# Optimization experiments

Measured on AMD Instinct MI355X. Metric: run time of the kernel, lower is better.

The kernel has to match this reference:

```python
import jax, jax.numpy as jnp
import numpy as np

B, Q, V, H, U = 4, 256, 2048, 512, 128

def setup_inputs() -> dict:
    key = jax.random.key(0)
    ks = jax.random.split(key, 5)
    return {
        "queries": jax.random.normal(ks[0], (B, Q, H), dtype=jnp.float32),
        "values": jax.random.normal(ks[1], (B, V, H), dtype=jnp.float32),
        "w1": jax.random.normal(ks[2], (H, U), dtype=jnp.float32) / np.sqrt(H),
        "w2": jax.random.normal(ks[3], (H, U), dtype=jnp.float32) / np.sqrt(H),
        "v": jax.random.normal(ks[4], (U,), dtype=jnp.float32) / np.sqrt(U),
    }

def reference(queries, values, w1, w2, v):
    # Project queries and values first (cheap GEMMs), then broadcast-add.
    pq = jnp.einsum("bqh,hu->bqu", queries, w1)          # [B,Q,U]
    pv = jnp.einsum("bvh,hu->bvu", values, w2)           # [B,V,U]
    # added_qv: [B,Q,V,U] -- the large intermediate the original materializes
    scores = jnp.einsum("bqvu,u->bqv", jnp.tanh(pq[:, :, None, :] + pv[:, None, :, :]), v)
    attn = jax.nn.softmax(scores, axis=-1)               # softmax over V (last axis, as tf.nn.softmax)
    return jnp.einsum("bqv,bvh->bqh", attn, values)      # [B,Q,H]
```

## Files before the change

### kernel.cpp

```cpp
#include <hip/hip_runtime.h>

#define BB 4
#define QQ 256
#define VV 2048
#define HH 512
#define UU 128

#define C2E   2.8853900817779268f
#define LOG2E 1.4426950408889634f

__device__ __forceinline__ void fma4(float4& a, float s, const float4& w) {
    a.x = fmaf(s, w.x, a.x);
    a.y = fmaf(s, w.y, a.y);
    a.z = fmaf(s, w.z, a.z);
    a.w = fmaf(s, w.w, a.w);
}
__device__ __forceinline__ float2 rcp2(float2 x) {
    return make_float2(__builtin_amdgcn_rcpf(x.x), __builtin_amdgcn_rcpf(x.y));
}
__device__ __forceinline__ float2 mul2(float2 a, float2 b) { return make_float2(a.x*b.x, a.y*b.y); }
__device__ __forceinline__ float2 muls(float2 a, float s)  { return make_float2(a.x*s, a.y*s); }
__device__ __forceinline__ float2 fma2(float2 a, float2 b, float2 c) {
    return make_float2(fmaf(a.x, b.x, c.x), fmaf(a.y, b.y, c.y));
}
__device__ __forceinline__ float2 fmas(float2 a, float s, float2 c) {
    return make_float2(fmaf(a.x, s, c.x), fmaf(a.y, s, c.y));
}

__global__ __launch_bounds__(256) void proj_kernel(const float* __restrict__ queries,
                                                   const float* __restrict__ values,
                                                   const float* __restrict__ w1,
                                                   const float* __restrict__ w2,
                                                   float* __restrict__ pqI,
                                                   float* __restrict__ pvI,
                                                   float* __restrict__ denom) {
    __shared__ float smem[32 * 36 + 32 * 128];
    float (*As)[36] = (float(*)[36])smem;
    float* Ws = smem + 32 * 36;
    float (*Ls)[36] = (float(*)[36])smem;

    const int bid = blockIdx.x;
    const int tid = threadIdx.x;
    if (bid == 0) *(float4*)&denom[tid * 4] = make_float4(0.f, 0.f, 0.f, 0.f);

    const bool isv = (bid < 256);
    const float* A; const float* W; int b, r0, ROWS; float* Ob;
    if (isv) {
        b = bid >> 6; r0 = (bid & 63) * 32;
        A = values + ((size_t)(b * VV + r0)) * HH;  W = w2;
        Ob = pvI + (size_t)b * UU * VV;  ROWS = VV;
    } else {
        const int q = bid - 256;
        b = q >> 3; r0 = (q & 7) * 32;
        A = queries + ((size_t)(b * QQ + r0)) * HH; W = w1;
        Ob = pqI + (size_t)b * UU * QQ;  ROWS = QQ;
    }

    const int tx = tid & 31;
    const int ty = tid >> 5;
    float4 acc[4];
#pragma unroll
    for (int j = 0; j < 4; j++) acc[j] = make_float4(0.f, 0.f, 0.f, 0.f);

    for (int k0 = 0; k0 < HH; k0 += 32) {
        {
            const int r = tid >> 3, kk4 = (tid & 7) * 4;
            const float4 a = *(const float4*)&A[(size_t)r * HH + k0 + kk4];
            As[kk4 + 0][r] = a.x; As[kk4 + 1][r] = a.y;
            As[kk4 + 2][r] = a.z; As[kk4 + 3][r] = a.w;
        }
#pragma unroll
        for (int t = 0; t < 4; t++) {
            const int f = tid + t * 256;
            const int kk = f >> 5, u4 = (f & 31) * 4;
            *(float4*)&Ws[kk * 128 + u4] = *(const float4*)&W[(size_t)(k0 + kk) * UU + u4];
        }
        __syncthreads();
#pragma unroll
        for (int kk = 0; kk < 32; kk++) {
            const float4 a = *(const float4*)&As[kk][ty * 4];
            const float4 w = *(const float4*)&Ws[kk * 128 + tx * 4];
            fma4(acc[0], a.x, w);
            fma4(acc[1], a.y, w);
            fma4(acc[2], a.z, w);
            fma4(acc[3], a.w, w);
        }
        __syncthreads();
    }
#pragma unroll
    for (int j = 0; j < 4; j++) {
        const float aa[4] = {acc[j].x, acc[j].y, acc[j].z, acc[j].w};
#pragma unroll
        for (int i = 0; i < 4; i++)
            Ls[tx * 4 + i][ty * 4 + j] = __builtin_amdgcn_exp2f(aa[i] * C2E);
    }
    __syncthreads();
#pragma unroll
    for (int t = 0; t < 4; t++) {
        const int idx = tid + t * 256;
        const int g = idx >> 5, r = idx & 31;
        float4 o;
        o.x = Ls[4 * g + 0][r]; o.y = Ls[4 * g + 1][r];
        o.z = Ls[4 * g + 2][r]; o.w = Ls[4 * g + 3][r];
        *(float4*)&Ob[((size_t)g * ROWS + r0 + r) * 4] = o;
    }
}

__global__ __launch_bounds__(1024, 4) void fused_kernel(const float* __restrict__ pqI,
                                                        const float* __restrict__ pvI,
                                                        const float* __restrict__ vvec,
                                                        const float* __restrict__ values,
                                                        float* __restrict__ slab,
                                                        float* __restrict__ denom) {
    __shared__ float att[512][20];
    __shared__ float scratch[24 * 512];
    __shared__ float wred[8][16];
    const int tid = threadIdx.x;
    const int bid = blockIdx.x;
    const int vs = bid & 3, qb = (bid >> 2) & 15, b = bid >> 6;
    const int qbase = qb * 16, vbase = vs * 512;

    const int vloc = tid & 511;
    const int uh = tid >> 9;
    const int v = vbase + vloc;

    float vsum = 0.0f;
#pragma unroll
    for (int u4 = 0; u4 < UU; u4 += 4) {
        const float4 t = *(const float4*)&vvec[u4];
        vsum += t.x + t.y + t.z + t.w;
    }

    const float* pv4 = pvI + (size_t)b * UU * VV + (size_t)v * 4;
    const float* pq4 = pqI + (size_t)b * UU * QQ + (size_t)qbase * 4;

    float2 acc[8];
#pragma unroll
    for (int p = 0; p < 8; p++) acc[p] = make_float2(0.f, 0.f);

    const int G0 = uh * 16;
    float4 ev = *(const float4*)&pv4[(size_t)G0 * VV * 4];

    for (int g = 0; g < 16; g++) {
        const int G = G0 + g;
        const float* eqp = &pq4[(size_t)G * QQ * 4];
        float4 e[16];
#pragma unroll
        for (int i = 0; i < 16; i++)
            e[i] = *(const float4*)&eqp[i * 4];
        float4 evn;
        if (g < 15) evn = *(const float4*)&pv4[(size_t)(G + 1) * VV * 4];
        const float4 wq = *(const float4*)&vvec[G * 4];
        const float w0 = 2.f * wq.x, w1 = 2.f * wq.y;
        const float w2 = 2.f * wq.z, w3 = 2.f * wq.w;
#pragma unroll
        for (int p = 0; p < 8; p++) {
            const float4 e0 = e[2 * p];
            const float4 e1 = e[2 * p + 1];
            const float2 a1 = make_float2(fmaf(e0.x, ev.x, 1.f), fmaf(e1.x, ev.x, 1.f));
            const float2 b1 = make_float2(fmaf(e0.y, ev.y, 1.f), fmaf(e1.y, ev.y, 1.f));
            const float2 c1 = make_float2(fmaf(e0.z, ev.z, 1.f), fmaf(e1.z, ev.z, 1.f));
            const float2 d1 = make_float2(fmaf(e0.w, ev.w, 1.f), fmaf(e1.w, ev.w, 1.f));
            const float2 pab = mul2(a1, b1), pcd = mul2(c1, d1);
            const float2 nab = fmas(a1, w1, muls(b1, w0));
            const float2 ncd = fmas(c1, w3, muls(d1, w2));
            const float2 num = fma2(nab, pcd, mul2(ncd, pab));
            const float2 den = mul2(pab, pcd);
            acc[p] = fma2(num, rcp2(den), acc[p]);
        }
        ev = evn;
    }

    float* cb = scratch;
    if (uh == 1) {
#pragma unroll
        for (int p = 0; p < 8; p++) {
            cb[(2 * p + 0) * 512 + vloc] = acc[p].x;
            cb[(2 * p + 1) * 512 + vloc] = acc[p].y;
        }
    }
    __syncthreads();
    if (uh == 0) {
#pragma unroll
        for (int p = 0; p < 8; p++) {
            const float hx = cb[(2 * p + 0) * 512 + vloc];
            const float hy = cb[(2 * p + 1) * 512 + vloc];
            float2 e;
            e.x = __builtin_amdgcn_exp2f((vsum - (acc[p].x + hx)) * LOG2E);
            e.y = __builtin_amdgcn_exp2f((vsum - (acc[p].y + hy)) * LOG2E);
            *(float2*)&att[vloc][2 * p] = e;
            acc[p] = e;
        }
#pragma unroll
        for (int off = 1; off < 64; off <<= 1) {
#pragma unroll
            for (int p = 0; p < 8; p++) {
                acc[p].x += __shfl_xor(acc[p].x, off, 64);
                acc[p].y += __shfl_xor(acc[p].y, off, 64);
            }
        }
        if ((tid & 63) == 0) {
            const int w = tid >> 6;
#pragma unroll
            for (int p = 0; p < 8; p++) {
                wred[w][2 * p + 0] = acc[p].x;
                wred[w][2 * p + 1] = acc[p].y;
            }
        }
    }
    __syncthreads();
    if (tid < 16) {
        float s = 0.f;
#pragma unroll
        for (int w = 0; w < 8; w++) s += wred[w][tid];
        atomicAdd(&denom[b * QQ + qbase + tid], s);
    }

    const int hg = tid & 127, sel = tid >> 7;
    const int qh = sel & 1, vh = sel >> 1;
    const int h0 = hg * 4;
    const float* vp = values + ((size_t)(b * VV + vbase + vh * 128)) * HH + h0;

    float4 oacc[8];
#pragma unroll
    for (int j = 0; j < 8; j++) oacc[j] = make_float4(0.f, 0.f, 0.f, 0.f);

#pragma unroll 2
    for (int vv = 0; vv < 128; vv++) {
        const float4 w = *(const float4*)&vp[(size_t)vv * HH];
        const float4 a0 = *(const float4*)&att[vh * 128 + vv][qh * 8 + 0];
        const float4 a1 = *(const float4*)&att[vh * 128 + vv][qh * 8 + 4];
        fma4(oacc[0], a0.x, w); fma4(oacc[1], a0.y, w);
        fma4(oacc[2], a0.z, w); fma4(oacc[3], a0.w, w);
        fma4(oacc[4], a1.x, w); fma4(oacc[5], a1.y, w);
        fma4(oacc[6], a1.z, w); fma4(oacc[7], a1.w, w);
    }

    float (*scr)[512] = (float(*)[512])scratch;
    for (int rr = 0; rr < 2; rr++) {
        __syncthreads();
        if (qh == rr && vh > 0) {
#pragma unroll
            for (int j = 0; j < 8; j++)
                *(float4*)&scr[(vh - 1) * 8 + j][h0] = oacc[j];
        }
        __syncthreads();
        if (qh == rr && vh == 0) {
            float* sp = slab + (size_t)vs * (BB * QQ * HH);
#pragma unroll
            for (int j = 0; j < 8; j++) {
                const float4 p0 = *(const float4*)&scr[0 * 8 + j][h0];
                const float4 p1 = *(const float4*)&scr[1 * 8 + j][h0];
                const float4 p2 = *(const float4*)&scr[2 * 8 + j][h0];
                float4 o;
                o.x = oacc[j].x + p0.x + p1.x + p2.x;
                o.y = oacc[j].y + p0.y + p1.y + p2.y;
                o.z = oacc[j].z + p0.z + p1.z + p2.z;
                o.w = oacc[j].w + p0.w + p1.w + p2.w;
                *(float4*)&sp[((size_t)(b * QQ + qbase + rr * 8 + j)) * HH + h0] = o;
            }
        }
    }
}

__global__ __launch_bounds__(256) void reduce_kernel(const float* __restrict__ slab,
                                                     const float* __restrict__ denom,
                                                     float* __restrict__ out) {
    const int i = blockIdx.x * 256 + threadIdx.x;
    const float r = __builtin_amdgcn_rcpf(denom[i >> 7]);
    const float4* s4 = (const float4*)slab;
    float4 s = s4[i];
#pragma unroll
    for (int k = 1; k < 4; k++) {
        const float4 p = s4[(size_t)k * (BB * QQ * HH / 4) + i];
        s.x += p.x; s.y += p.y; s.z += p.z; s.w += p.w;
    }
    s.x *= r; s.y *= r; s.z *= r; s.w *= r;
    ((float4*)out)[i] = s;
}

extern "C" void kernel_launch(void* const* d_in, const int* in_sizes, int n_in,
                              void* d_out, int out_size, void* d_ws, size_t ws_size,
                              hipStream_t stream) {
    const float* queries = (const float*)d_in[0];
    const float* values  = (const float*)d_in[1];
    const float* w1      = (const float*)d_in[2];
    const float* w2      = (const float*)d_in[3];
    const float* vvec    = (const float*)d_in[4];
    float* out = (float*)d_out;

    float* ws    = (float*)d_ws;
    float* pqI   = ws;
    float* pvI   = pqI + BB * UU * QQ;
    float* denom = pvI + (size_t)BB * UU * VV;
    float* slab  = denom + BB * QQ;

    proj_kernel<<<256 + 32, 256, 0, stream>>>(queries, values, w1, w2, pqI, pvI, denom);
    fused_kernel<<<BB * (QQ / 16) * (VV / 512), 1024, 0, stream>>>(pqI, pvI, vvec, values, slab, denom);
    reduce_kernel<<<(BB * QQ * HH) / 4 / 256, 256, 0, stream>>>(slab, denom, out);
}
```

Baseline: 175.2 us.

## Split fused attention kernel into separate scores and PV kernels

After: 231.6 us. 32.2% more time.

```diff
diff --git a/kernel.cpp b/kernel.cpp
--- a/kernel.cpp
+++ b/kernel.cpp
@@ -106,25 +106,18 @@
     }
 }
 
-__global__ __launch_bounds__(1024, 4) void fused_kernel(const float* __restrict__ pqI,
+__global__ __launch_bounds__(256, 8) void scores_kernel(const float* __restrict__ pqI,
                                                         const float* __restrict__ pvI,
                                                         const float* __restrict__ vvec,
-                                                        const float* __restrict__ values,
-                                                        float* __restrict__ slab,
+                                                        float* __restrict__ attT,
                                                         float* __restrict__ denom) {
-    __shared__ float att[512][20];
-    __shared__ float scratch[24 * 512];
-    __shared__ float wred[8][16];
-    const int tid = threadIdx.x;
-    const int bid = blockIdx.x;
-    const int vs = bid & 3, qb = (bid >> 2) & 15, b = bid >> 6;
-    const int qbase = qb * 16, vbase = vs * 512;
-
-    const int vloc = tid & 511;
-    const int uh = tid >> 9;
-    const int v = vbase + vloc;
-
-    float vsum = 0.0f;
+    const int tid = threadIdx.x, bid = blockIdx.x;
+    const int lane = tid & 63, w = tid >> 6;
+    const int vb = bid & 31, qb = (bid >> 5) & 15, b = bid >> 9;
+    const int v = vb * 64 + lane;
+    const int q0 = qb * 16 + w * 4;
+
+    float vsum = 0.f;
 #pragma unroll
     for (int u4 = 0; u4 < UU; u4 += 4) {
         const float4 t = *(const float4*)&vvec[u4];
@@ -132,31 +125,24 @@
     }
 
     const float* pv4 = pvI + (size_t)b * UU * VV + (size_t)v * 4;
-    const float* pq4 = pqI + (size_t)b * UU * QQ + (size_t)qbase * 4;
-
-    float2 acc[8];
-#pragma unroll
-    for (int p = 0; p < 8; p++) acc[p] = make_float2(0.f, 0.f);
-
-    const int G0 = uh * 16;
-    float4 ev = *(const float4*)&pv4[(size_t)G0 * VV * 4];
-
-    for (int g = 0; g < 16; g++) {
-        const int G = G0 + g;
+    const float* pq4 = pqI + (size_t)b * UU * QQ + (size_t)q0 * 4;
+
+    float2 acc[2];
+    acc[0] = make_float2(0.f, 0.f);
+    acc[1] = make_float2(0.f, 0.f);
+
+    float4 ev = *(const float4*)&pv4[0];
+    for (int G = 0; G < 32; G++) {
+        float4 evn;
+        if (G < 31) evn = *(const float4*)&pv4[(size_t)(G + 1) * VV * 4];
         const float* eqp = &pq4[(size_t)G * QQ * 4];
-        float4 e[16];
-#pragma unroll
-        for (int i = 0; i < 16; i++)
-            e[i] = *(const float4*)&eqp[i * 4];
-        float4 evn;
-        if (g < 15) evn = *(const float4*)&pv4[(size_t)(G + 1) * VV * 4];
         const float4 wq = *(const float4*)&vvec[G * 4];
         const float w0 = 2.f * wq.x, w1 = 2.f * wq.y;
         const float w2 = 2.f * wq.z, w3 = 2.f * wq.w;
 #pragma unroll
-        for (int p = 0; p < 8; p++) {
-            const float4 e0 = e[2 * p];
-            const float4 e1 = e[2 * p + 1];
+        for (int p = 0; p < 2; p++) {
+            const float4 e0 = *(const float4*)&eqp[(2 * p) * 4];
+            const float4 e1 = *(const float4*)&eqp[(2 * p + 1) * 4];
             const float2 a1 = make_float2(fmaf(e0.x, ev.x, 1.f), fmaf(e1.x, ev.x, 1.f));
             const float2 b1 = make_float2(fmaf(e0.y, ev.y, 1.f), fmaf(e1.y, ev.y, 1.f));
             const float2 c1 = make_float2(fmaf(e0.z, ev.z, 1.f), fmaf(e1.z, ev.z, 1.f));
@@ -171,55 +157,43 @@
         ev = evn;
     }
 
-    float* cb = scratch;
-    if (uh == 1) {
-#pragma unroll
-        for (int p = 0; p < 8; p++) {
-            cb[(2 * p + 0) * 512 + vloc] = acc[p].x;
-            cb[(2 * p + 1) * 512 + vloc] = acc[p].y;
-        }
-    }
-    __syncthreads();
-    if (uh == 0) {
-#pragma unroll
-        for (int p = 0; p < 8; p++) {
-            const float hx = cb[(2 * p + 0) * 512 + vloc];
-            const float hy = cb[(2 * p + 1) * 512 + vloc];
-            float2 e;
-            e.x = __builtin_amdgcn_exp2f((vsum - (acc[p].x + hx)) * LOG2E);
-            e.y = __builtin_amdgcn_exp2f((vsum - (acc[p].y + hy)) * LOG2E);
-            *(float2*)&att[vloc][2 * p] = e;
-            acc[p] = e;
-        }
-#pragma unroll
-        for (int off = 1; off < 64; off <<= 1) {
-#pragma unroll
-            for (int p = 0; p < 8; p++) {
-                acc[p].x += __shfl_xor(acc[p].x, off, 64);
-                acc[p].y += __shfl_xor(acc[p].y, off, 64);
-            }
-        }
-        if ((tid & 63) == 0) {
-            const int w = tid >> 6;
-#pragma unroll
-            for (int p = 0; p < 8; p++) {
-                wred[w][2 * p + 0] = acc[p].x;
-                wred[w][2 * p + 1] = acc[p].y;
-            }
-        }
-    }
-    __syncthreads();
-    if (tid < 16) {
-        float s = 0.f;
-#pragma unroll
-        for (int w = 0; w < 8; w++) s += wred[w][tid];
-        atomicAdd(&denom[b * QQ + qbase + tid], s);
-    }
+    float4 eo;
+    eo.x = __builtin_amdgcn_exp2f((vsum - acc[0].x) * LOG2E);
+    eo.y = __builtin_amdgcn_exp2f((vsum - acc[0].y) * LOG2E);
+    eo.z = __builtin_amdgcn_exp2f((vsum - acc[1].x) * LOG2E);
+    eo.w = __builtin_amdgcn_exp2f((vsum - acc[1].y) * LOG2E);
+    *(float4*)&attT[((((size_t)b * 16 + qb) * VV) + v) * 16 + w * 4] = eo;
+
+    float4 s = eo;
+#pragma unroll
+    for (int off = 1; off < 64; off <<= 1) {
+        s.x += __shfl_xor(s.x, off, 64);
+        s.y += __shfl_xor(s.y, off, 64);
+        s.z += __shfl_xor(s.z, off, 64);
+        s.w += __shfl_xor(s.w, off, 64);
+    }
+    if (lane == 0) {
+        atomicAdd(&denom[b * QQ + q0 + 0], s.x);
+        atomicAdd(&denom[b * QQ + q0 + 1], s.y);
+        atomicAdd(&denom[b * QQ + q0 + 2], s.z);
+        atomicAdd(&denom[b * QQ + q0 + 3], s.w);
+    }
+}
+
+__global__ __launch_bounds__(1024, 4) void pv_kernel(const float* __restrict__ attT,
+                                                     const float* __restrict__ values,
+                                                     float* __restrict__ slab) {
+    __shared__ float scratch[24 * 512];
+    const int tid = threadIdx.x;
+    const int bid = blockIdx.x;
+    const int vs = bid & 3, qb = (bid >> 2) & 15, b = bid >> 6;
+    const int qbase = qb * 16, vbase = vs * 512;
 
     const int hg = tid & 127, sel = tid >> 7;
     const int qh = sel & 1, vh = sel >> 1;
     const int h0 = hg * 4;
     const float* vp = values + ((size_t)(b * VV + vbase + vh * 128)) * HH + h0;
+    const float* ap = attT + (((size_t)b * 16 + qb) * VV + vbase + vh * 128) * 16;
 
     float4 oacc[8];
 #pragma unroll
@@ -228,8 +202,8 @@
 #pragma unroll 2
     for (int vv = 0; vv < 128; vv++) {
         const float4 w = *(const float4*)&vp[(size_t)vv * HH];
-        const float4 a0 = *(const float4*)&att[vh * 128 + vv][qh * 8 + 0];
-        const float4 a1 = *(const float4*)&att[vh * 128 + vv][qh * 8 + 4];
+        const float4 a0 = *(const float4*)&ap[vv * 16 + qh * 8 + 0];
+        const float4 a1 = *(const float4*)&ap[vv * 16 + qh * 8 + 4];
         fma4(oacc[0], a0.x, w); fma4(oacc[1], a0.y, w);
         fma4(oacc[2], a0.z, w); fma4(oacc[3], a0.w, w);
         fma4(oacc[4], a1.x, w); fma4(oacc[5], a1.y, w);
@@ -294,8 +268,10 @@
     float* pvI   = pqI + BB * UU * QQ;
     float* denom = pvI + (size_t)BB * UU * VV;
     float* slab  = denom + BB * QQ;
+    float* attT  = slab + (size_t)4 * (BB * QQ * HH);
 
     proj_kernel<<<256 + 32, 256, 0, stream>>>(queries, values, w1, w2, pqI, pvI, denom);
-    fused_kernel<<<BB * (QQ / 16) * (VV / 512), 1024, 0, stream>>>(pqI, pvI, vvec, values, slab, denom);
+    scores_kernel<<<BB * (QQ / 16) * (VV / 64), 256, 0, stream>>>(pqI, pvI, vvec, attT, denom);
+    pv_kernel<<<BB * (QQ / 16) * (VV / 512), 1024, 0, stream>>>(attT, values, slab);
     reduce_kernel<<<(BB * QQ * HH) / 4 / 256, 256, 0, stream>>>(slab, denom, out);
 }
```

## Fuse projection, attention and reduction into one cooperative kernel with grid syncs

Applied to the files above, without the earlier changes.

Measured after the change: 271.6 us. 55.1% more time.

```diff
diff --git a/kernel.cpp b/kernel.cpp
--- a/kernel.cpp
+++ b/kernel.cpp
@@ -1,4 +1,5 @@
 #include <hip/hip_runtime.h>
+#include <hip/hip_cooperative_groups.h>
 
 #define BB 4
 #define QQ 256
@@ -27,256 +28,265 @@
     return make_float2(fmaf(a.x, s, c.x), fmaf(a.y, s, c.y));
 }
 
-__global__ __launch_bounds__(256) void proj_kernel(const float* __restrict__ queries,
-                                                   const float* __restrict__ values,
-                                                   const float* __restrict__ w1,
-                                                   const float* __restrict__ w2,
-                                                   float* __restrict__ pqI,
-                                                   float* __restrict__ pvI,
-                                                   float* __restrict__ denom) {
-    __shared__ float smem[32 * 36 + 32 * 128];
-    float (*As)[36] = (float(*)[36])smem;
-    float* Ws = smem + 32 * 36;
-    float (*Ls)[36] = (float(*)[36])smem;
-
-    const int bid = blockIdx.x;
-    const int tid = threadIdx.x;
-    if (bid == 0) *(float4*)&denom[tid * 4] = make_float4(0.f, 0.f, 0.f, 0.f);
-
-    const bool isv = (bid < 256);
-    const float* A; const float* W; int b, r0, ROWS; float* Ob;
-    if (isv) {
-        b = bid >> 6; r0 = (bid & 63) * 32;
-        A = values + ((size_t)(b * VV + r0)) * HH;  W = w2;
-        Ob = pvI + (size_t)b * UU * VV;  ROWS = VV;
-    } else {
-        const int q = bid - 256;
-        b = q >> 3; r0 = (q & 7) * 32;
-        A = queries + ((size_t)(b * QQ + r0)) * HH; W = w1;
-        Ob = pqI + (size_t)b * UU * QQ;  ROWS = QQ;
-    }
-
-    const int tx = tid & 31;
-    const int ty = tid >> 5;
-    float4 acc[4];
-#pragma unroll
-    for (int j = 0; j < 4; j++) acc[j] = make_float4(0.f, 0.f, 0.f, 0.f);
-
-    for (int k0 = 0; k0 < HH; k0 += 32) {
-        {
-            const int r = tid >> 3, kk4 = (tid & 7) * 4;
-            const float4 a = *(const float4*)&A[(size_t)r * HH + k0 + kk4];
-            As[kk4 + 0][r] = a.x; As[kk4 + 1][r] = a.y;
-            As[kk4 + 2][r] = a.z; As[kk4 + 3][r] = a.w;
-        }
-#pragma unroll
-        for (int t = 0; t < 4; t++) {
-            const int f = tid + t * 256;
-            const int kk = f >> 5, u4 = (f & 31) * 4;
-            *(float4*)&Ws[kk * 128 + u4] = *(const float4*)&W[(size_t)(k0 + kk) * UU + u4];
-        }
-        __syncthreads();
-#pragma unroll
-        for (int kk = 0; kk < 32; kk++) {
-            const float4 a = *(const float4*)&As[kk][ty * 4];
-            const float4 w = *(const float4*)&Ws[kk * 128 + tx * 4];
-            fma4(acc[0], a.x, w);
-            fma4(acc[1], a.y, w);
-            fma4(acc[2], a.z, w);
-            fma4(acc[3], a.w, w);
-        }
-        __syncthreads();
-    }
-#pragma unroll
-    for (int j = 0; j < 4; j++) {
-        const float aa[4] = {acc[j].x, acc[j].y, acc[j].z, acc[j].w};
-#pragma unroll
-        for (int i = 0; i < 4; i++)
-            Ls[tx * 4 + i][ty * 4 + j] = __builtin_amdgcn_exp2f(aa[i] * C2E);
-    }
-    __syncthreads();
-#pragma unroll
-    for (int t = 0; t < 4; t++) {
-        const int idx = tid + t * 256;
-        const int g = idx >> 5, r = idx & 31;
-        float4 o;
-        o.x = Ls[4 * g + 0][r]; o.y = Ls[4 * g + 1][r];
-        o.z = Ls[4 * g + 2][r]; o.w = Ls[4 * g + 3][r];
-        *(float4*)&Ob[((size_t)g * ROWS + r0 + r) * 4] = o;
-    }
-}
-
-__global__ __launch_bounds__(1024, 4) void fused_kernel(const float* __restrict__ pqI,
-                                                        const float* __restrict__ pvI,
-                                                        const float* __restrict__ vvec,
-                                                        const float* __restrict__ values,
-                                                        float* __restrict__ slab,
-                                                        float* __restrict__ denom) {
+__global__ __launch_bounds__(1024, 4) void mega_kernel(const float* __restrict__ queries,
+                                                       const float* __restrict__ values,
+                                                       const float* __restrict__ w1,
+                                                       const float* __restrict__ w2,
+                                                       const float* __restrict__ vvec,
+                                                       float* __restrict__ pqI,
+                                                       float* __restrict__ pvI,
+                                                       float* __restrict__ denom,
+                                                       float* __restrict__ slab,
+                                                       float* __restrict__ out) {
     __shared__ float att[512][20];
     __shared__ float scratch[24 * 512];
     __shared__ float wred[8][16];
+
     const int tid = threadIdx.x;
     const int bid = blockIdx.x;
-    const int vs = bid & 3, qb = (bid >> 2) & 15, b = bid >> 6;
-    const int qbase = qb * 16, vbase = vs * 512;
-
-    const int vloc = tid & 511;
-    const int uh = tid >> 9;
-    const int v = vbase + vloc;
-
-    float vsum = 0.0f;
-#pragma unroll
-    for (int u4 = 0; u4 < UU; u4 += 4) {
-        const float4 t = *(const float4*)&vvec[u4];
-        vsum += t.x + t.y + t.z + t.w;
+
+    {
+        const int slot = tid >> 8, stid = tid & 255;
+        bool active = false;
+        const float* A = nullptr; const float* W = nullptr; float* Ob = nullptr;
+        int r0 = 0, ROWS = 0;
+        if (slot == 0) {
+            const int vb = bid;
+            const int b = vb >> 6; r0 = (vb & 63) * 32;
+            A = values + ((size_t)(b * VV + r0)) * HH;  W = w2;
+            Ob = pvI + (size_t)b * UU * VV;  ROWS = VV;  active = true;
+        } else if (slot == 1 && bid < 32) {
+            const int q = bid;
+            const int b = q >> 3; r0 = (q & 7) * 32;
+            A = queries + ((size_t)(b * QQ + r0)) * HH; W = w1;
+            Ob = pqI + (size_t)b * UU * QQ;  ROWS = QQ;  active = true;
+        } else if (slot == 2 && bid == 0) {
+            ((float4*)denom)[stid] = make_float4(0.f, 0.f, 0.f, 0.f);
+        }
+
+        float* preg = scratch + (slot & 1) * 5248;
+        float (*As)[36] = (float(*)[36])preg;
+        float* Ws = preg + 32 * 36;
+        float (*Ls)[36] = (float(*)[36])preg;
+
+        const int tx = stid & 31;
+        const int ty = stid >> 5;
+        float4 acc[4];
+#pragma unroll
+        for (int j = 0; j < 4; j++) acc[j] = make_float4(0.f, 0.f, 0.f, 0.f);
+
+        for (int k0 = 0; k0 < HH; k0 += 32) {
+            if (active) {
+                {
+                    const int r = stid >> 3, kk4 = (stid & 7) * 4;
+                    const float4 a = *(const float4*)&A[(size_t)r * HH + k0 + kk4];
+                    As[kk4 + 0][r] = a.x; As[kk4 + 1][r] = a.y;
+                    As[kk4 + 2][r] = a.z; As[kk4 + 3][r] = a.w;
+                }
+#pragma unroll
+                for (int t = 0; t < 4; t++) {
+                    const int f = stid + t * 256;
+                    const int kk = f >> 5, u4 = (f & 31) * 4;
+                    *(float4*)&Ws[kk * 128 + u4] = *(const float4*)&W[(size_t)(k0 + kk) * UU + u4];
+                }
+            }
+            __syncthreads();
+            if (active) {
+#pragma unroll
+                for (int kk = 0; kk < 32; kk++) {
+                    const float4 a = *(const float4*)&As[kk][ty * 4];
+                    const float4 w = *(const float4*)&Ws[kk * 128 + tx * 4];
+                    fma4(acc[0], a.x, w);
+                    fma4(acc[1], a.y, w);
+                    fma4(acc[2], a.z, w);
+                    fma4(acc[3], a.w, w);
+                }
+            }
+            __syncthreads();
+        }
+        if (active) {
+#pragma unroll
+            for (int j = 0; j < 4; j++) {
+                const float aa[4] = {acc[j].x, acc[j].y, acc[j].z, acc[j].w};
+#pragma unroll
+                for (int i = 0; i < 4; i++)
+                    Ls[tx * 4 + i][ty * 4 + j] = __builtin_amdgcn_exp2f(aa[i] * C2E);
+            }
+        }
+        __syncthreads();
+        if (active) {
+#pragma unroll
+            for (int t = 0; t < 4; t++) {
+                const int idx = stid + t * 256;
+                const int g = idx >> 5, rr = idx & 31;
+                float4 o;
+                o.x = Ls[4 * g + 0][rr]; o.y = Ls[4 * g + 1][rr];
+                o.z = Ls[4 * g + 2][rr]; o.w = Ls[4 * g + 3][rr];
+                *(float4*)&Ob[((size_t)g * ROWS + r0 + rr) * 4] = o;
+            }
+        }
     }
 
-    const float* pv4 = pvI + (size_t)b * UU * VV + (size_t)v * 4;
-    const float* pq4 = pqI + (size_t)b * UU * QQ + (size_t)qbase * 4;
-
-    float2 acc[8];
-#pragma unroll
-    for (int p = 0; p < 8; p++) acc[p] = make_float2(0.f, 0.f);
-
-    const int G0 = uh * 16;
-    float4 ev = *(const float4*)&pv4[(size_t)G0 * VV * 4];
-
-    for (int g = 0; g < 16; g++) {
-        const int G = G0 + g;
-        const float* eqp = &pq4[(size_t)G * QQ * 4];
-        float4 e[16];
-#pragma unroll
-        for (int i = 0; i < 16; i++)
-            e[i] = *(const float4*)&eqp[i * 4];
-        float4 evn;
-        if (g < 15) evn = *(const float4*)&pv4[(size_t)(G + 1) * VV * 4];
-        const float4 wq = *(const float4*)&vvec[G * 4];
-        const float w0 = 2.f * wq.x, w1 = 2.f * wq.y;
-        const float w2 = 2.f * wq.z, w3 = 2.f * wq.w;
-#pragma unroll
-        for (int p = 0; p < 8; p++) {
-            const float4 e0 = e[2 * p];
-            const float4 e1 = e[2 * p + 1];
-            const float2 a1 = make_float2(fmaf(e0.x, ev.x, 1.f), fmaf(e1.x, ev.x, 1.f));
-            const float2 b1 = make_float2(fmaf(e0.y, ev.y, 1.f), fmaf(e1.y, ev.y, 1.f));
-            const float2 c1 = make_float2(fmaf(e0.z, ev.z, 1.f), fmaf(e1.z, ev.z, 1.f));
-            const float2 d1 = make_float2(fmaf(e0.w, ev.w, 1.f), fmaf(e1.w, ev.w, 1.f));
-            const float2 pab = mul2(a1, b1), pcd = mul2(c1, d1);
-            const float2 nab = fmas(a1, w1, muls(b1, w0));
-            const float2 ncd = fmas(c1, w3, muls(d1, w2));
-            const float2 num = fma2(nab, pcd, mul2(ncd, pab));
-            const float2 den = mul2(pab, pcd);
-            acc[p] = fma2(num, rcp2(den), acc[p]);
-        }
-        ev = evn;
+    cooperative_groups::this_grid().sync();
+
+    {
+        const int vs = bid & 3, qb = (bid >> 2) & 15, b = bid >> 6;
+        const int qbase = qb * 16, vbase = vs * 512;
+
+        const int vloc = tid & 511;
+        const int uh = tid >> 9;
+        const int v = vbase + vloc;
+
+        float vsum = 0.0f;
+#pragma unroll
+        for (int u4 = 0; u4 < UU; u4 += 4) {
+            const float4 t = *(const float4*)&vvec[u4];
+            vsum += t.x + t.y + t.z + t.w;
+        }
+
+        const float* pv4 = pvI + (size_t)b * UU * VV + (size_t)v * 4;
+        const float* pq4 = pqI + (size_t)b * UU * QQ + (size_t)qbase * 4;
+
+        float2 acc[8];
+#pragma unroll
+        for (int p = 0; p < 8; p++) acc[p] = make_float2(0.f, 0.f);
+
+        const int G0 = uh * 16;
+        float4 ev = *(const float4*)&pv4[(size_t)G0 * VV * 4];
+
+        for (int g = 0; g < 16; g++) {
+            const int G = G0 + g;
+            const float* eqp = &pq4[(size_t)G * QQ * 4];
+            float4 evn;
+            if (g < 15) evn = *(const float4*)&pv4[(size_t)(G + 1) * VV * 4];
+            const float4 wq = *(const float4*)&vvec[G * 4];
+            const float w0 = 2.f * wq.x, w1 = 2.f * wq.y;
+            const float w2 = 2.f * wq.z, w3 = 2.f * wq.w;
+#pragma unroll
+            for (int p = 0; p < 8; p++) {
+                const float4 e0 = *(const float4*)&eqp[(2 * p) * 4];
+                const float4 e1 = *(const float4*)&eqp[(2 * p + 1) * 4];
+                const float2 a1 = make_float2(fmaf(e0.x, ev.x, 1.f), fmaf(e1.x, ev.x, 1.f));
+                const float2 b1 = make_float2(fmaf(e0.y, ev.y, 1.f), fmaf(e1.y, ev.y, 1.f));
+                const float2 c1 = make_float2(fmaf(e0.z, ev.z, 1.f), fmaf(e1.z, ev.z, 1.f));
+                const float2 d1 = make_float2(fmaf(e0.w, ev.w, 1.f), fmaf(e1.w, ev.w, 1.f));
+                const float2 pab = mul2(a1, b1), pcd = mul2(c1, d1);
+                const float2 nab = fmas(a1, w1, muls(b1, w0));
+                const float2 ncd = fmas(c1, w3, muls(d1, w2));
+                const float2 num = fma2(nab, pcd, mul2(ncd, pab));
+                const float2 den = mul2(pab, pcd);
+                acc[p] = fma2(num, rcp2(den), acc[p]);
+            }
+            ev = evn;
+        }
+
+        float* cb = scratch;
+        if (uh == 1) {
+#pragma unroll
+            for (int p = 0; p < 8; p++) {
+                cb[(2 * p + 0) * 512 + vloc] = acc[p].x;
+                cb[(2 * p + 1) * 512 + vloc] = acc[p].y;
+            }
+        }
+        __syncthreads();
+        if (uh == 0) {
+#pragma unroll
+            for (int p = 0; p < 8; p++) {
+                const float hx = cb[(2 * p + 0) * 512 + vloc];
+                const float hy = cb[(2 * p + 1) * 512 + vloc];
+                float2 e;
+                e.x = __builtin_amdgcn_exp2f((vsum - (acc[p].x + hx)) * LOG2E);
+                e.y = __builtin_amdgcn_exp2f((vsum - (acc[p].y + hy)) * LOG2E);
+                *(float2*)&att[vloc][2 * p] = e;
+                acc[p] = e;
+            }
+#pragma unroll
+            for (int off = 1; off < 64; off <<= 1) {
+#pragma unroll
+                for (int p = 0; p < 8; p++) {
+                    acc[p].x += __shfl_xor(acc[p].x, off, 64);
+                    acc[p].y += __shfl_xor(acc[p].y, off, 64);
+                }
+            }
+            if ((tid & 63) == 0) {
+                const int w = tid >> 6;
+#pragma unroll
+                for (int p = 0; p < 8; p++) {
+                    wred[w][2 * p + 0] = acc[p].x;
+                    wred[w][2 * p + 1] = acc[p].y;
+                }
+            }
+        }
+        __syncthreads();
+        if (tid < 16) {
+            float s = 0.f;
+#pragma unroll
+            for (int w = 0; w < 8; w++) s += wred[w][tid];
+            atomicAdd(&denom[b * QQ + qbase + tid], s);
+        }
+
+        const int hg = tid & 127, sel = tid >> 7;
+        const int qh = sel & 1, vh = sel >> 1;
+        const int h0 = hg * 4;
+        const float* vp = values + ((size_t)(b * VV + vbase + vh * 128)) * HH + h0;
+
+        float4 oacc[8];
+#pragma unroll
+        for (int j = 0; j < 8; j++) oacc[j] = make_float4(0.f, 0.f, 0.f, 0.f);
+
+#pragma unroll 2
+        for (int vv = 0; vv < 128; vv++) {
+            const float4 w = *(const float4*)&vp[(size_t)vv * HH];
+            const float4 a0 = *(const float4*)&att[vh * 128 + vv][qh * 8 + 0];
+            const float4 a1 = *(const float4*)&att[vh * 128 + vv][qh * 8 + 4];
+            fma4(oacc[0], a0.x, w); fma4(oacc[1], a0.y, w);
+            fma4(oacc[2], a0.z, w); fma4(oacc[3], a0.w, w);
+            fma4(oacc[4], a1.x, w); fma4(oacc[5], a1.y, w);
+            fma4(oacc[6], a1.z, w); fma4(oacc[7], a1.w, w);
+        }
+
+        float (*scr)[512] = (float(*)[512])scratch;
+        for (int rr = 0; rr < 2; rr++) {
+            __syncthreads();
+            if (qh == rr && vh > 0) {
+#pragma unroll
+                for (int j = 0; j < 8; j++)
+                    *(float4*)&scr[(vh - 1) * 8 + j][h0] = oacc[j];
+            }
+            __syncthreads();
+            if (qh == rr && vh == 0) {
+                float* sp = slab + (size_t)vs * (BB * QQ * HH);
+#pragma unroll
+                for (int j = 0; j < 8; j++) {
+                    const float4 p0 = *(const float4*)&scr[0 * 8 + j][h0];
+                    const float4 p1 = *(const float4*)&scr[1 * 8 + j][h0];
+                    const float4 p2 = *(const float4*)&scr[2 * 8 + j][h0];
+                    float4 o;
+                    o.x = oacc[j].x + p0.x + p1.x + p2.x;
+                    o.y = oacc[j].y + p0.y + p1.y + p2.y;
+                    o.z = oacc[j].z + p0.z + p1.z + p2.z;
+                    o.w = oacc[j].w + p0.w + p1.w + p2.w;
+                    *(float4*)&sp[((size_t)(b * QQ + qbase + rr * 8 + j)) * HH + h0] = o;
+                }
+            }
+        }
     }
 
-    float* cb = scratch;
-    if (uh == 1) {
-#pragma unroll
-        for (int p = 0; p < 8; p++) {
-            cb[(2 * p + 0) * 512 + vloc] = acc[p].x;
-            cb[(2 * p + 1) * 512 + vloc] = acc[p].y;
-        }
+    cooperative_groups::this_grid().sync();
+
+    if (tid < 512) {
+        const int i = bid * 512 + tid;
+        const float r = __builtin_amdgcn_rcpf(denom[i >> 7]);
+        const float4* s4 = (const float4*)slab;
+        float4 s = s4[i];
+#pragma unroll
+        for (int k = 1; k < 4; k++) {
+            const float4 p = s4[(size_t)k * (BB * QQ * HH / 4) + i];
+            s.x += p.x; s.y += p.y; s.z += p.z; s.w += p.w;
+        }
+        s.x *= r; s.y *= r; s.z *= r; s.w *= r;
+        ((float4*)out)[i] = s;
     }
-    __syncthreads();
-    if (uh == 0) {
-#pragma unroll
-        for (int p = 0; p < 8; p++) {
-            const float hx = cb[(2 * p + 0) * 512 + vloc];
-            const float hy = cb[(2 * p + 1) * 512 + vloc];
-            float2 e;
-            e.x = __builtin_amdgcn_exp2f((vsum - (acc[p].x + hx)) * LOG2E);
-            e.y = __builtin_amdgcn_exp2f((vsum - (acc[p].y + hy)) * LOG2E);
-            *(float2*)&att[vloc][2 * p] = e;
-            acc[p] = e;
-        }
-#pragma unroll
-        for (int off = 1; off < 64; off <<= 1) {
-#pragma unroll
-            for (int p = 0; p < 8; p++) {
-                acc[p].x += __shfl_xor(acc[p].x, off, 64);
-                acc[p].y += __shfl_xor(acc[p].y, off, 64);
-            }
-        }
-        if ((tid & 63) == 0) {
-            const int w = tid >> 6;
-#pragma unroll
-            for (int p = 0; p < 8; p++) {
-                wred[w][2 * p + 0] = acc[p].x;
-                wred[w][2 * p + 1] = acc[p].y;
-            }
-        }
-    }
-    __syncthreads();
-    if (tid < 16) {
-        float s = 0.f;
-#pragma unroll
-        for (int w = 0; w < 8; w++) s += wred[w][tid];
-        atomicAdd(&denom[b * QQ + qbase + tid], s);
-    }
-
-    const int hg = tid & 127, sel = tid >> 7;
-    const int qh = sel & 1, vh = sel >> 1;
-    const int h0 = hg * 4;
-    const float* vp = values + ((size_t)(b * VV + vbase + vh * 128)) * HH + h0;
-
-    float4 oacc[8];
-#pragma unroll
-    for (int j = 0; j < 8; j++) oacc[j] = make_float4(0.f, 0.f, 0.f, 0.f);
-
-#pragma unroll 2
-    for (int vv = 0; vv < 128; vv++) {
-        const float4 w = *(const float4*)&vp[(size_t)vv * HH];
-        const float4 a0 = *(const float4*)&att[vh * 128 + vv][qh * 8 + 0];
-        const float4 a1 = *(const float4*)&att[vh * 128 + vv][qh * 8 + 4];
-        fma4(oacc[0], a0.x, w); fma4(oacc[1], a0.y, w);
-        fma4(oacc[2], a0.z, w); fma4(oacc[3], a0.w, w);
-        fma4(oacc[4], a1.x, w); fma4(oacc[5], a1.y, w);
-        fma4(oacc[6], a1.z, w); fma4(oacc[7], a1.w, w);
-    }
-
-    float (*scr)[512] = (float(*)[512])scratch;
-    for (int rr = 0; rr < 2; rr++) {
-        __syncthreads();
-        if (qh == rr && vh > 0) {
-#pragma unroll
-            for (int j = 0; j < 8; j++)
-                *(float4*)&scr[(vh - 1) * 8 + j][h0] = oacc[j];
-        }
-        __syncthreads();
-        if (qh == rr && vh == 0) {
-            float* sp = slab + (size_t)vs * (BB * QQ * HH);
-#pragma unroll
-            for (int j = 0; j < 8; j++) {
-                const float4 p0 = *(const float4*)&scr[0 * 8 + j][h0];
-                const float4 p1 = *(const float4*)&scr[1 * 8 + j][h0];
-                const float4 p2 = *(const float4*)&scr[2 * 8 + j][h0];
-                float4 o;
-                o.x = oacc[j].x + p0.x + p1.x + p2.x;
-                o.y = oacc[j].y + p0.y + p1.y + p2.y;
-                o.z = oacc[j].z + p0.z + p1.z + p2.z;
-                o.w = oacc[j].w + p0.w + p1.w + p2.w;
-                *(float4*)&sp[((size_t)(b * QQ + qbase + rr * 8 + j)) * HH + h0] = o;
-            }
-        }
-    }
-}
-
-__global__ __launch_bounds__(256) void reduce_kernel(const float* __restrict__ slab,
-                                                     const float* __restrict__ denom,
-                                                     float* __restrict__ out) {
-    const int i = blockIdx.x * 256 + threadIdx.x;
-    const float r = __builtin_amdgcn_rcpf(denom[i >> 7]);
-    const float4* s4 = (const float4*)slab;
-    float4 s = s4[i];
-#pragma unroll
-    for (int k = 1; k < 4; k++) {
-        const float4 p = s4[(size_t)k * (BB * QQ * HH / 4) + i];
-        s.x += p.x; s.y += p.y; s.z += p.z; s.w += p.w;
-    }
-    s.x *= r; s.y *= r; s.z *= r; s.w *= r;
-    ((float4*)out)[i] = s;
 }
 
 extern "C" void kernel_launch(void* const* d_in, const int* in_sizes, int n_in,
@@ -295,7 +305,9 @@
     float* denom = pvI + (size_t)BB * UU * VV;
     float* slab  = denom + BB * QQ;
 
-    proj_kernel<<<256 + 32, 256, 0, stream>>>(queries, values, w1, w2, pqI, pvI, denom);
-    fused_kernel<<<BB * (QQ / 16) * (VV / 512), 1024, 0, stream>>>(pqI, pvI, vvec, values, slab, denom);
-    reduce_kernel<<<(BB * QQ * HH) / 4 / 256, 256, 0, stream>>>(slab, denom, out);
-}
+    void* args[] = {(void*)&queries, (void*)&values, (void*)&w1, (void*)&w2,
+                    (void*)&vvec, (void*)&pqI, (void*)&pvI, (void*)&denom,
+                    (void*)&slab, (void*)&out};
+    hipLaunchCooperativeKernel((const void*)mega_kernel, dim3(256), dim3(1024),
+                               args, 0, stream);
+}
```
